# Performance work log

Measured on AMD Instinct MI355X. Metric: run time of the kernel, lower is better.

Reference implementation:

```python
import jax, jax.numpy as jnp
import numpy as np

B, L, K, D, S = 8, 1024, 1024, 128, 16  # batch, nodes, eigvecs, d_model(=d_inner), d_state
ABAR_EPS = 1e-3
BN_EPS = 1e-5


def setup_inputs() -> dict:
    key = jax.random.key(0)
    ks = jax.random.split(key, 10)
    x = jax.random.normal(ks[0], (B, L, D), jnp.float32)
    attn_mask = jnp.ones((B, L), jnp.bool_)
    EigVecs = jax.random.normal(ks[1], (B, L, K), jnp.float32)
    EigVals = jax.random.uniform(ks[2], (B, K), jnp.float32)
    # BatchNorm1d (eval mode) params
    bn_gamma = jnp.ones((D,), jnp.float32)
    bn_beta = jnp.zeros((D,), jnp.float32)
    bn_mean = jnp.zeros((D,), jnp.float32)
    bn_var = jnp.ones((D,), jnp.float32)
    # in_proj Linear(D, 2*D)
    W_in = jax.random.normal(ks[3], (D, 2 * D), jnp.float32) / np.float32(np.sqrt(D))
    b_in = jnp.zeros((2 * D,), jnp.float32)
    # SSM params
    log_Delta = np.float32(np.log(1e-3)) + np.float32(np.log(0.1) - np.log(1e-3)) * jax.random.uniform(ks[4], (1, D), jnp.float32)
    Bp = 0.01 * jax.random.normal(ks[5], (1, D, S), jnp.float32)
    Cp = 0.01 * jax.random.normal(ks[6], (1, D, S), jnp.float32)
    log_A_real = jnp.log(0.5 * jnp.ones((D, S), jnp.float32))
    A_imag = jnp.pi * jnp.broadcast_to(jnp.arange(D, dtype=jnp.float32)[:, None], (D, S))
    # out_proj Linear(D, D)
    W_out = jax.random.normal(ks[7], (D, D), jnp.float32) / np.float32(np.sqrt(D))
    b_out = jnp.zeros((D,), jnp.float32)
    return {
        "x": x, "attn_mask": attn_mask, "EigVecs": EigVecs, "EigVals": EigVals,
        "bn_gamma": bn_gamma, "bn_beta": bn_beta, "bn_mean": bn_mean, "bn_var": bn_var,
        "W_in": W_in, "b_in": b_in, "log_Delta": log_Delta, "Bp": Bp, "Cp": Cp,
        "log_A_real": log_A_real, "A_imag": A_imag, "W_out": W_out, "b_out": b_out,
    }


def reference(x, attn_mask, EigVecs, EigVals, bn_gamma, bn_beta, bn_mean, bn_var,
              W_in, b_in, log_Delta, Bp, Cp, log_A_real, A_imag, W_out, b_out):
    # --- eig preprocessing ---
    ev = 1.0 - EigVals[:, :, None, None]            # (B,K,1,1)
    ev = jnp.nan_to_num(ev)
    Q = jnp.nan_to_num(EigVecs)                      # (B,L,K)
    Q = Q / jnp.linalg.norm(Q, axis=-1, keepdims=True)
    Q = jnp.nan_to_num(Q)
    # --- in_proj: BatchNorm1d (eval) + Linear ---
    xb = (x - bn_mean) * (bn_gamma / jnp.sqrt(bn_var + BN_EPS)) + bn_beta
    h = xb @ W_in + b_in                             # (B,L,2D)
    x1, z = jnp.split(h, 2, axis=-1)                 # split [d_model, d_model]
    u = x1 * jax.nn.silu(z)                          # (B,L,D)
    # --- discretized SSM params ---
    delta = jnp.exp(log_Delta)                       # (1,D)
    A = -jnp.exp(log_A_real) + 1j * A_imag           # (D,S) complex
    Abar = jnp.exp(-ABAR_EPS + delta[..., None] * A) # (1,D,S) complex
    Bbar = delta[..., None] * Bp                     # (1,D,S)
    # --- graph Fourier transform ---
    QTX = jnp.einsum('blk,bld->bkd', Q, u)           # (B,K,D)
    QTXB = QTX[..., None] * Bbar                     # (B,K,D,S)
    lamA = ev * Abar[:, None]                        # (B,K,D,S) complex
    lamQ = jnp.real(lamA / (1.0 - lamA) * QTXB)      # A_complex & not BC_complex -> .real
    # --- inverse transform + C reduction (fused) ---
    yssm = jnp.einsum('blk,bkds,ds->bld', Q, lamQ, Cp[0])  # (B,L,D)
    y = jax.nn.silu(yssm) @ W_out + b_out
    return y
```

## Files before the change

kernel.cpp:

```cpp
#include <hip/hip_runtime.h>
#include <math.h>

#define B_ 8
#define L_ 1024
#define K_ 1024
#define D_ 128
#define S_ 16
#define DS_ (D_ * S_)
#define NIT_ 16

typedef short bf16x8 __attribute__((ext_vector_type(8)));
typedef float f32x4 __attribute__((ext_vector_type(4)));
typedef __attribute__((address_space(1))) const unsigned int gu32;
typedef __attribute__((address_space(3))) unsigned int lu32;

__device__ inline unsigned short f2bf(float f) {
    unsigned int u = __float_as_uint(f);
    u = (u + 0x7fffu + ((u >> 16) & 1u)) >> 16;
    return (unsigned short)u;
}
__device__ inline float bf2f(unsigned short h) {
    return __uint_as_float(((unsigned int)h) << 16);
}

__device__ inline size_t bswz(int b, int c, int n) {
    return ((((size_t)b * 32 + (c >> 5)) * 4 + ((c >> 3) & 3)) * 128 + n) * 8;
}

__global__ __launch_bounds__(256) void k_pre(
    const float* __restrict__ E, const float* __restrict__ x,
    const float* __restrict__ g, const float* __restrict__ beta,
    const float* __restrict__ mean, const float* __restrict__ var,
    const float* __restrict__ W_in, const float* __restrict__ b_in,
    const float* __restrict__ log_Delta, const float* __restrict__ Bp,
    const float* __restrict__ Cp, const float* __restrict__ log_A_real,
    const float* __restrict__ A_imag, const float* __restrict__ W_out,
    float* __restrict__ rn_out, float* __restrict__ par,
    unsigned short* __restrict__ woH, unsigned short* __restrict__ woL,
    unsigned short* __restrict__ uswH, unsigned short* __restrict__ uswL) {
    __shared__ unsigned short xbh[4][16][32], xbl[4][16][32];
    __shared__ float szs[16][132];
    __shared__ float us[16][132];
    __shared__ float rsum[16];
    __shared__ float rnS[16];
    int bx = blockIdx.x;
    int row0 = bx * 16;
    int t = threadIdx.x;
    if (bx < 8) {
        int i = bx * 256 + t;
        int d = i >> 4, s = i & 15;
        double delta = exp((double)log_Delta[d]);
        double Are = -exp((double)log_A_real[i]);
        double Aim = (double)A_imag[i];
        double mag = exp(-1e-3 + delta * Are);
        double ang = delta * Aim;
        int o = s * D_ + d;
        par[o]           = (float)(mag * cos(ang));
        par[DS_ + o]     = (float)(mag * sin(ang));
        par[2 * DS_ + o] = (float)(delta * (double)Bp[i] * (double)Cp[i]);
    }
    if (bx >= 8 && bx < 12) {
        int kc = bx - 8;
        #pragma unroll
        for (int j = 0; j < 16; ++j) {
            int s = t * 16 + j;
            int ws = s >> 10, nt = (s >> 9) & 1, ln = (s >> 3) & 63, ii = s & 7;
            int row = kc * 32 + (ln >> 4) * 8 + ii;
            int col = ws * 32 + nt * 16 + (ln & 15);
            float wv = W_out[row * 128 + col];
            unsigned short h = f2bf(wv);
            woH[kc * 4096 + s] = h;
            woL[kc * 4096 + s] = f2bf(wv - bf2f(h));
        }
    }
    {
        int r = t >> 4, tt = t & 15;
        const float4* Ep = (const float4*)(E + (size_t)(row0 + r) * K_);
        float s = 0.f;
        #pragma unroll
        for (int i = 0; i < 16; ++i) {
            float4 v = Ep[tt + i * 16];
            s += v.x * v.x + v.y * v.y + v.z * v.z + v.w * v.w;
        }
        s += __shfl_xor(s, 8, 64);
        s += __shfl_xor(s, 4, 64);
        s += __shfl_xor(s, 2, 64);
        s += __shfl_xor(s, 1, 64);
        if (tt == 0) rsum[r] = s;
    }
    #pragma unroll
    for (int p = 0; p < 8; ++p) {
        int idx = t + p * 256;
        int dd = idx & 127, r = idx >> 7;
        float sc = g[dd] / sqrtf(var[dd] + 1e-5f);
        float v = (x[(size_t)(row0 + r) * D_ + dd] - mean[dd]) * sc + beta[dd];
        unsigned short h = f2bf(v);
        xbh[dd >> 5][r][dd & 31] = h;
        xbl[dd >> 5][r][dd & 31] = f2bf(v - bf2f(h));
    }
    __syncthreads();
    if (t < 16) {
        float rv = 1.0f / sqrtf(rsum[t]);
        rnS[t] = rv;
        rn_out[row0 + t] = rv;
    }
    __syncthreads();
    int wave = t >> 6, lane = t & 63;
    int fr = lane & 15, q = lane >> 4;
    f32x4 acc[4];
    #pragma unroll
    for (int ct = 0; ct < 4; ++ct) acc[ct] = (f32x4){0.f, 0.f, 0.f, 0.f};
    #pragma unroll
    for (int c = 0; c < 4; ++c) {
        bf16x8 ah = *(const bf16x8*)&xbh[c][fr][q * 8];
        bf16x8 al = *(const bf16x8*)&xbl[c][fr][q * 8];
        #pragma unroll
        for (int ct = 0; ct < 4; ++ct) {
            int col = wave * 64 + ct * 16 + fr;
            bf16x8 bh, bl;
            #pragma unroll
            for (int i = 0; i < 8; ++i) {
                float wv = W_in[(c * 32 + q * 8 + i) * 256 + col];
                unsigned short h = f2bf(wv);
                bh[i] = (short)h;
                bl[i] = (short)f2bf(wv - bf2f(h));
            }
            acc[ct] = __builtin_amdgcn_mfma_f32_16x16x32_bf16(ah, bh, acc[ct], 0, 0, 0);
            acc[ct] = __builtin_amdgcn_mfma_f32_16x16x32_bf16(ah, bl, acc[ct], 0, 0, 0);
            acc[ct] = __builtin_amdgcn_mfma_f32_16x16x32_bf16(al, bh, acc[ct], 0, 0, 0);
        }
    }
    if (wave >= 2) {
        #pragma unroll
        for (int ct = 0; ct < 4; ++ct) {
            int cz = (wave - 2) * 64 + ct * 16 + fr;
            float b2v = b_in[128 + cz];
            #pragma unroll
            for (int r = 0; r < 4; ++r) {
                float z = acc[ct][r] + b2v;
                float sig = 1.0f / (1.0f + __expf(-z));
                szs[q * 4 + r][cz] = z * sig;
            }
        }
    }
    __syncthreads();
    if (wave < 2) {
        #pragma unroll
        for (int ct = 0; ct < 4; ++ct) {
            int cx = wave * 64 + ct * 16 + fr;
            float b1v = b_in[cx];
            #pragma unroll
            for (int r = 0; r < 4; ++r) {
                int row = q * 4 + r;
                float x1 = acc[ct][r] + b1v;
                us[row][cx] = rnS[row] * x1 * szs[row][cx];
            }
        }
    }
    __syncthreads();
    int j = t & 127, half = t >> 7;
    bf16x8 hv, lv;
    #pragma unroll
    for (int r = 0; r < 8; ++r) {
        float uv = us[half * 8 + r][j];
        unsigned short h = f2bf(uv);
        hv[r] = (short)h;
        lv[r] = (short)f2bf(uv - bf2f(h));
    }
    int b = row0 >> 10;
    int l0 = (row0 & 1023) + half * 8;
    size_t off = bswz(b, l0, j);
    *(bf16x8*)&uswH[off] = hv;
    *(bf16x8*)&uswL[off] = lv;
}

#define STAGE_B(itS, nb)                                                        \
    _Pragma("unroll")                                                           \
    for (int j2 = 0; j2 < 4; ++j2) {                                            \
        int s = wave * 4 + j2;                         \
        int cts = s >> 4, s2 = s & 15;                                          \
        int qq = s2 & 3, nh = (s2 >> 2) & 1, hl = s2 >> 3;                      \
        size_t src0 = (size_t)((itS) * 2 + cts) * 4096;                         \
        const unsigned short* src =                                             \
            (hl ? BbL : BbH) + src0 + ((size_t)qq * 128 + nh * 64 + lane) * 8;  \
        unsigned short* dst =                                                   \
            (hl ? &sBl[nb][cts][0] : &sBh[nb][cts][0]) + qq * 1032 + nh * 512;  \
        __builtin_amdgcn_global_load_lds((gu32*)src, (lu32*)dst, 16, 0, 0);     \
    }

#define G1_WRITE_A(nb, v0, v1, v2, v3)                                           \
    {                                                                            \
        unsigned short h0 = f2bf(v0), h1 = f2bf(v1);                             \
        unsigned short l0 = f2bf((v0) - bf2f(h0)), l1 = f2bf((v1) - bf2f(h1));   \
        *(unsigned int*)&sAh[nb][0][aoff] = (unsigned)h0 | ((unsigned)h1 << 16); \
        *(unsigned int*)&sAl[nb][0][aoff] = (unsigned)l0 | ((unsigned)l1 << 16); \
        unsigned short h2 = f2bf(v2), h3 = f2bf(v3);                             \
        unsigned short l2 = f2bf((v2) - bf2f(h2)), l3 = f2bf((v3) - bf2f(h3));   \
        *(unsigned int*)&sAh[nb][1][aoff] = (unsigned)h2 | ((unsigned)h3 << 16); \
        *(unsigned int*)&sAl[nb][1][aoff] = (unsigned)l2 | ((unsigned)l3 << 16); \
    }

#define MFMA_PHASE(aB, cB)                                                       \
    {                                                                            \
        __builtin_amdgcn_s_setprio(1);                                           \
        bf16x8 ah[2], al[2], bh[2], bl[2];                                       \
        _Pragma("unroll")                                                        \
        for (int mt = 0; mt < 2; ++mt) {                                         \
            int row = mt * 16 + fr;                                              \
            int p = (q + (row >> 3)) & 3;                                        \
            int offA = row * 40 + p * 8;                                         \
            ah[mt] = *(const bf16x8*)&sAh[aB][kh][offA];                         \
            al[mt] = *(const bf16x8*)&sAl[aB][kh][offA];                         \
        }                                                                        \
        _Pragma("unroll")                                                        \
        for (int nt = 0; nt < 2; ++nt) {                                         \
            int offB = q * 1032 + (wn + nt * 16 + fr) * 8;                       \
            bh[nt] = *(const bf16x8*)&sBh[cB][kh][offB];                         \
            bl[nt] = *(const bf16x8*)&sBl[cB][kh][offB];                         \
        }                                                                        \
        _Pragma("unroll")                                                        \
        for (int mt = 0; mt < 2; ++mt)                                           \
            _Pragma("unroll")                                                    \
            for (int nt = 0; nt < 2; ++nt) {                                     \
                acc[mt][nt] = __builtin_amdgcn_mfma_f32_16x16x32_bf16(ah[mt], bh[nt], acc[mt][nt], 0, 0, 0); \
                acc[mt][nt] = __builtin_amdgcn_mfma_f32_16x16x32_bf16(ah[mt], bl[nt], acc[mt][nt], 0, 0, 0); \
                acc[mt][nt] = __builtin_amdgcn_mfma_f32_16x16x32_bf16(al[mt], bh[nt], acc[mt][nt], 0, 0, 0); \
            }                                                                    \
        __builtin_amdgcn_s_setprio(0);                                           \
    }

__global__ __launch_bounds__(512, 2) void k_g1(
    const float* __restrict__ E,
    const unsigned short* __restrict__ BH, const unsigned short* __restrict__ BL,
    const float* __restrict__ EigVals, const float* __restrict__ par,
    unsigned short* __restrict__ GswH, unsigned short* __restrict__ GswL) {
    __shared__ alignas(16) unsigned short sAh[2][2][1280], sAl[2][2][1280];
    __shared__ alignas(16) unsigned short sBh[3][2][4128], sBl[3][2][4128];
    __shared__ float evS[32];
    int bx = blockIdx.x;
    int b = bx & 7;
    int m0 = (bx >> 3) * 32;
    const float* Ab = E + (size_t)b * (1024 * 1024);
    const unsigned short* BbH = BH + (size_t)b * 131072;
    const unsigned short* BbL = BL + (size_t)b * 131072;
    int t = threadIdx.x;
    int wave = t >> 6, lane = t & 63;
    int fr = lane & 15, q = lane >> 4;
    int kh = wave & 1;
    int wn = (wave >> 1) * 32;
    int am = t & 31, jj = t >> 5;
    int ag = jj >> 2;
    int arot = (ag + (am >> 3)) & 3;
    int aoff = am * 40 + arot * 8 + ((2 * jj) & 7);
    if (t < 32) evS[t] = 1.0f - EigVals[b * 1024 + m0 + t];
    f32x4 acc[2][2];
    #pragma unroll
    for (int mt = 0; mt < 2; ++mt)
        #pragma unroll
        for (int nt = 0; nt < 2; ++nt)
            acc[mt][nt] = (f32x4){0.f, 0.f, 0.f, 0.f};

    {
        STAGE_B(0, 0);
        STAGE_B(1, 1);
        float v0 = Ab[(size_t)(2 * jj) * 1024 + m0 + am];
        float v1 = Ab[(size_t)(2 * jj + 1) * 1024 + m0 + am];
        float v2 = Ab[(size_t)(32 + 2 * jj) * 1024 + m0 + am];
        float v3 = Ab[(size_t)(32 + 2 * jj + 1) * 1024 + m0 + am];
        G1_WRITE_A(0, v0, v1, v2, v3);
        asm volatile("s_waitcnt vmcnt(0) lgkmcnt(0)" ::: "memory");
        __builtin_amdgcn_s_barrier();
        asm volatile("" ::: "memory");
    }

    for (int it = 0; it < NIT_; ++it) {
        int cB = it % 3;
        int fB = (it + 2) % 3;
        int aB = it & 1, naB = aB ^ 1;
        float v0 = 0.f, v1 = 0.f, v2 = 0.f, v3 = 0.f;
        if (it + 1 < NIT_) {
            int cb = (it + 1) * 64;
            v0 = Ab[(size_t)(cb + 2 * jj) * 1024 + m0 + am];
            v1 = Ab[(size_t)(cb + 2 * jj + 1) * 1024 + m0 + am];
            v2 = Ab[(size_t)(cb + 32 + 2 * jj) * 1024 + m0 + am];
            v3 = Ab[(size_t)(cb + 32 + 2 * jj + 1) * 1024 + m0 + am];
        }
        if (it + 2 < NIT_) STAGE_B(it + 2, fB);
        MFMA_PHASE(aB, cB)
        if (it + 1 < NIT_) G1_WRITE_A(naB, v0, v1, v2, v3);
        asm volatile("s_waitcnt lgkmcnt(0)" ::: "memory");
        __builtin_amdgcn_s_barrier();
        asm volatile("" ::: "memory");
    }

    float (*Gs)[132] = (float (*)[132])(&sBh[0][0][0]);
    if (kh == 0) {
        #pragma unroll
        for (int mt = 0; mt < 2; ++mt)
            #pragma unroll
            for (int nt = 0; nt < 2; ++nt) {
                int col = wn + nt * 16 + fr;
                #pragma unroll
                for (int r = 0; r < 4; ++r)
                    Gs[mt * 16 + q * 4 + r][col] = acc[mt][nt][r];
            }
    }
    __syncthreads();
    if (kh == 1) {
        #pragma unroll
        for (int mt = 0; mt < 2; ++mt)
            #pragma unroll
            for (int nt = 0; nt < 2; ++nt) {
                int col = wn + nt * 16 + fr;
                #pragma unroll
                for (int r = 0; r < 4; ++r)
                    Gs[mt * 16 + q * 4 + r][col] += acc[mt][nt][r];
            }
    }
    __syncthreads();
    {
        int col = t & 127, rowg = t >> 7;
        float arr[S_], aii[S_], ccc[S_];
        #pragma unroll
        for (int ss = 0; ss < S_; ++ss) {
            arr[ss] = par[ss * D_ + col];
            aii[ss] = par[DS_ + ss * D_ + col];
            ccc[ss] = par[2 * DS_ + ss * D_ + col];
        }
        #pragma unroll
        for (int i = 0; i < 8; ++i) {
            int row = rowg * 8 + i;
            float ev = evS[row];
            float w = 0.f;
            #pragma unroll
            for (int ss = 0; ss < S_; ++ss) {
                float a = ev * arr[ss], bi = ev * aii[ss];
                float oma = 1.0f - a;
                float b2 = bi * bi;
                float num = fmaf(a, oma, -b2);
                float den = fmaf(oma, oma, b2);
                float rr = __builtin_amdgcn_rcpf(den);
                rr = rr * (2.0f - den * rr);
                w = fmaf(ccc[ss], num * rr, w);
            }
            Gs[row][col] *= w;
        }
    }
    __syncthreads();
    {
        int d = t & 127, kg = t >> 7;
        bf16x8 hv, lv;
        #pragma unroll
        for (int i = 0; i < 8; ++i) {
            float v = Gs[kg * 8 + i][d];
            unsigned short h = f2bf(v);
            hv[i] = (short)h;
            lv[i] = (short)f2bf(v - bf2f(h));
        }
        int ct = m0 >> 5;
        size_t off = (((size_t)(b * 32 + ct) * 4 + kg) * 128 + d) * 8;
        *(bf16x8*)&GswH[off] = hv;
        *(bf16x8*)&GswL[off] = lv;
    }
}

#define G2_WRITE_A(nb, va)                                                       \
    {                                                                            \
        unsigned short h0 = f2bf((va).x), h1 = f2bf((va).y);                     \
        unsigned short h2 = f2bf((va).z), h3 = f2bf((va).w);                     \
        unsigned short l0 = f2bf((va).x - bf2f(h0)), l1 = f2bf((va).y - bf2f(h1));\
        unsigned short l2 = f2bf((va).z - bf2f(h2)), l3 = f2bf((va).w - bf2f(h3));\
        *(uint2*)&sAh[nb][chunk][aoff] =                                         \
            (uint2){(unsigned)h0 | ((unsigned)h1 << 16),                         \
                    (unsigned)h2 | ((unsigned)h3 << 16)};                        \
        *(uint2*)&sAl[nb][chunk][aoff] =                                         \
            (uint2){(unsigned)l0 | ((unsigned)l1 << 16),                         \
                    (unsigned)l2 | ((unsigned)l3 << 16)};                        \
    }

__global__ __launch_bounds__(512, 2) void k_g2(
    const float* __restrict__ E,
    const unsigned short* __restrict__ BH, const unsigned short* __restrict__ BL,
    const float* __restrict__ rn,
    const unsigned short* __restrict__ woH, const unsigned short* __restrict__ woL,
    const float* __restrict__ b_out, float* __restrict__ y) {
    __shared__ alignas(16) unsigned short sAh[2][2][1280], sAl[2][2][1280];
    __shared__ alignas(16) unsigned short sBh[3][2][4128], sBl[3][2][4128];
    __shared__ float rnS[32];
    int bx = blockIdx.x;
    int b = bx & 7;
    int m0 = (bx >> 3) * 32;
    const float* Ab = E + (size_t)b * (1024 * 1024);
    const unsigned short* BbH = BH + (size_t)b * 131072;
    const unsigned short* BbL = BL + (size_t)b * 131072;
    int t = threadIdx.x;
    int wave = t >> 6, lane = t & 63;
    int fr = lane & 15, q = lane >> 4;
    int kh = wave & 1;
    int wn = (wave >> 1) * 32;
    int am = t >> 4, c4 = (t & 15) * 4;
    int chunk = c4 >> 5, cw = c4 & 31;
    int ag = cw >> 3;
    int arot = (ag + (am >> 3)) & 3;
    int aoff = am * 40 + arot * 8 + (cw & 7);
    if (t < 32) rnS[t] = rn[b * 1024 + m0 + t];
    f32x4 acc[2][2];
    #pragma unroll
    for (int mt = 0; mt < 2; ++mt)
        #pragma unroll
        for (int nt = 0; nt < 2; ++nt)
            acc[mt][nt] = (f32x4){0.f, 0.f, 0.f, 0.f};

    {
        STAGE_B(0, 0);
        STAGE_B(1, 1);
        float4 va = *(const float4*)&Ab[(size_t)(m0 + am) * 1024 + c4];
        G2_WRITE_A(0, va);
        asm volatile("s_waitcnt vmcnt(0) lgkmcnt(0)" ::: "memory");
        __builtin_amdgcn_s_barrier();
        asm volatile("" ::: "memory");
    }

    for (int it = 0; it < NIT_; ++it) {
        int cB = it % 3;
        int fB = (it + 2) % 3;
        int aB = it & 1, naB = aB ^ 1;
        float4 va = (float4){0.f, 0.f, 0.f, 0.f};
        if (it + 1 < NIT_)
            va = *(const float4*)&Ab[(size_t)(m0 + am) * 1024 + (it + 1) * 64 + c4];
        if (it + 2 < NIT_) STAGE_B(it + 2, fB);
        MFMA_PHASE(aB, cB)
        if (it + 1 < NIT_) G2_WRITE_A(naB, va);
        asm volatile("s_waitcnt lgkmcnt(0)" ::: "memory");
        __builtin_amdgcn_s_barrier();
        asm volatile("" ::: "memory");
    }

    float (*Ysf)[132] = (float (*)[132])(&sBh[0][0][0]);
    if (kh == 0) {
        #pragma unroll
        for (int mt = 0; mt < 2; ++mt)
            #pragma unroll
            for (int nt = 0; nt < 2; ++nt) {
                int col = wn + nt * 16 + fr;
                #pragma unroll
                for (int r = 0; r < 4; ++r)
                    Ysf[mt * 16 + q * 4 + r][col] = acc[mt][nt][r];
            }
    }
    __syncthreads();
    if (kh == 1) {
        #pragma unroll
        for (int mt = 0; mt < 2; ++mt)
            #pragma unroll
            for (int nt = 0; nt < 2; ++nt) {
                int col = wn + nt * 16 + fr;
                #pragma unroll
                for (int r = 0; r < 4; ++r)
                    Ysf[mt * 16 + q * 4 + r][col] += acc[mt][nt][r];
            }
    }
    __syncthreads();
    unsigned short (*ysh)[32][40] = (unsigned short (*)[32][40])(&sBl[0][0][0]);
    unsigned short (*ysl)[32][40] = (unsigned short (*)[32][40])(&sBl[0][0][0] + 5120);
    {
        int col = t & 127, rowg = t >> 7;
        #pragma unroll
        for (int i = 0; i < 8; ++i) {
            int row = rowg * 8 + i;
            float v = Ysf[row][col] * rnS[row];
            float sig = 1.0f / (1.0f + __expf(-v));
            float u = v * sig;
            unsigned short h = f2bf(u);
            ysh[col >> 5][row][col & 31] = h;
            ysl[col >> 5][row][col & 31] = f2bf(u - bf2f(h));
        }
    }
    __syncthreads();
    {
        int mh = wave & 1, ws = wave >> 1;
        const bf16x8* WH = (const bf16x8*)woH;
        const bf16x8* WL = (const bf16x8*)woL;
        f32x4 a2[2];
        a2[0] = (f32x4){0.f, 0.f, 0.f, 0.f};
        a2[1] = (f32x4){0.f, 0.f, 0.f, 0.f};
        #pragma unroll
        for (int kc = 0; kc < 4; ++kc) {
            bf16x8 ah = *(const bf16x8*)&ysh[kc][mh * 16 + fr][q * 8];
            bf16x8 al = *(const bf16x8*)&ysl[kc][mh * 16 + fr][q * 8];
            #pragma unroll
            for (int nt = 0; nt < 2; ++nt) {
                bf16x8 bh = WH[((kc * 4 + ws) * 2 + nt) * 64 + lane];
                bf16x8 bl = WL[((kc * 4 + ws) * 2 + nt) * 64 + lane];
                a2[nt] = __builtin_amdgcn_mfma_f32_16x16x32_bf16(ah, bh, a2[nt], 0, 0, 0);
                a2[nt] = __builtin_amdgcn_mfma_f32_16x16x32_bf16(ah, bl, a2[nt], 0, 0, 0);
                a2[nt] = __builtin_amdgcn_mfma_f32_16x16x32_bf16(al, bh, a2[nt], 0, 0, 0);
            }
        }
        #pragma unroll
        for (int nt = 0; nt < 2; ++nt) {
            int col = ws * 32 + nt * 16 + fr;
            float bo = b_out[col];
            #pragma unroll
            for (int r = 0; r < 4; ++r) {
                int row = mh * 16 + q * 4 + r;
                y[((size_t)b * 1024 + m0 + row) * 128 + col] = a2[nt][r] + bo;
            }
        }
    }
}

extern "C" void kernel_launch(void* const* d_in, const int* in_sizes, int n_in,
                              void* d_out, int out_size, void* d_ws, size_t ws_size,
                              hipStream_t stream) {
    const float* x          = (const float*)d_in[0];
    const float* EigVecs    = (const float*)d_in[2];
    const float* EigVals    = (const float*)d_in[3];
    const float* bn_gamma   = (const float*)d_in[4];
    const float* bn_beta    = (const float*)d_in[5];
    const float* bn_mean    = (const float*)d_in[6];
    const float* bn_var     = (const float*)d_in[7];
    const float* W_in       = (const float*)d_in[8];
    const float* b_in       = (const float*)d_in[9];
    const float* log_Delta  = (const float*)d_in[10];
    const float* Bp         = (const float*)d_in[11];
    const float* Cp         = (const float*)d_in[12];
    const float* log_A_real = (const float*)d_in[13];
    const float* A_imag     = (const float*)d_in[14];
    const float* W_out      = (const float*)d_in[15];
    const float* b_out      = (const float*)d_in[16];

    float* y = (float*)d_out;
    char* w = (char*)d_ws;
    float* rn            = (float*)(w);
    float* par           = (float*)(w + 32768);
    unsigned short* woH  = (unsigned short*)(w + 57344);
    unsigned short* woL  = (unsigned short*)(w + 90112);
    unsigned short* uswH = (unsigned short*)(w + 131072);
    unsigned short* uswL = (unsigned short*)(w + 131072 + (1u << 21));
    unsigned short* GswH = (unsigned short*)(w + 131072 + 2 * (1u << 21));
    unsigned short* GswL = (unsigned short*)(w + 131072 + 3 * (1u << 21));

    k_pre<<<dim3(B_ * L_ / 16), dim3(256), 0, stream>>>(
        EigVecs, x, bn_gamma, bn_beta, bn_mean, bn_var, W_in, b_in,
        log_Delta, Bp, Cp, log_A_real, A_imag, W_out, rn, par, woH, woL,
        uswH, uswL);
    k_g1<<<dim3(256), dim3(512), 0, stream>>>(
        EigVecs, uswH, uswL, EigVals, par, GswH, GswL);
    k_g2<<<dim3(256), dim3(512), 0, stream>>>(
        EigVecs, GswH, GswL, rn, woH, woL, b_out, y);
}
```

Baseline: 154.5 us.

## Pre-split W_in to bf16 hi/lo once and pair rational terms in weight

Adds a small kernel that converts W_in into pre-swizzled bf16 high/low fragments once per call. k_pre then loads these fragments directly instead of having each of its 512 blocks reload and split the fp32 weights. Separately, the per-state rational weight sum is rewritten so two terms share one reciprocal, using num = oma - den, which halves the rcp and Newton-step work. The cost is an extra kernel launch, extra workspace, and slightly different rounding in the weight sum.

```diff
diff --git a/kernel.cpp b/kernel.cpp
--- a/kernel.cpp
+++ b/kernel.cpp
@@ -27,11 +27,32 @@
     return ((((size_t)b * 32 + (c >> 5)) * 4 + ((c >> 3) & 3)) * 128 + n) * 8;
 }
 
+__global__ __launch_bounds__(256) void k_w(
+    const float* __restrict__ W_in,
+    unsigned short* __restrict__ wiH, unsigned short* __restrict__ wiL) {
+    int g = blockIdx.x * 256 + threadIdx.x;
+    int lane = g & 63, rest = g >> 6;
+    int ct = rest & 3, wv = (rest >> 2) & 3, c = rest >> 4;
+    int rbase = c * 32 + (lane >> 4) * 8;
+    int col = wv * 64 + ct * 16 + (lane & 15);
+    bf16x8 hv, lv;
+    #pragma unroll
+    for (int i = 0; i < 8; ++i) {
+        float wvl = W_in[(rbase + i) * 256 + col];
+        unsigned short h = f2bf(wvl);
+        hv[i] = (short)h;
+        lv[i] = (short)f2bf(wvl - bf2f(h));
+    }
+    *(bf16x8*)&wiH[(size_t)g * 8] = hv;
+    *(bf16x8*)&wiL[(size_t)g * 8] = lv;
+}
+
 __global__ __launch_bounds__(256) void k_pre(
     const float* __restrict__ E, const float* __restrict__ x,
     const float* __restrict__ g, const float* __restrict__ beta,
     const float* __restrict__ mean, const float* __restrict__ var,
-    const float* __restrict__ W_in, const float* __restrict__ b_in,
+    const unsigned short* __restrict__ wiH, const unsigned short* __restrict__ wiL,
+    const float* __restrict__ b_in,
     const float* __restrict__ log_Delta, const float* __restrict__ Bp,
     const float* __restrict__ Cp, const float* __restrict__ log_A_real,
     const float* __restrict__ A_imag, const float* __restrict__ W_out,
@@ -107,6 +128,8 @@
     __syncthreads();
     int wave = t >> 6, lane = t & 63;
     int fr = lane & 15, q = lane >> 4;
+    const bf16x8* WIH = (const bf16x8*)wiH;
+    const bf16x8* WIL = (const bf16x8*)wiL;
     f32x4 acc[4];
     #pragma unroll
     for (int ct = 0; ct < 4; ++ct) acc[ct] = (f32x4){0.f, 0.f, 0.f, 0.f};
@@ -116,15 +139,9 @@
         bf16x8 al = *(const bf16x8*)&xbl[c][fr][q * 8];
         #pragma unroll
         for (int ct = 0; ct < 4; ++ct) {
-            int col = wave * 64 + ct * 16 + fr;
-            bf16x8 bh, bl;
-            #pragma unroll
-            for (int i = 0; i < 8; ++i) {
-                float wv = W_in[(c * 32 + q * 8 + i) * 256 + col];
-                unsigned short h = f2bf(wv);
-                bh[i] = (short)h;
-                bl[i] = (short)f2bf(wv - bf2f(h));
-            }
+            int idx = ((c * 4 + wave) * 4 + ct) * 64 + lane;
+            bf16x8 bh = WIH[idx];
+            bf16x8 bl = WIL[idx];
             acc[ct] = __builtin_amdgcn_mfma_f32_16x16x32_bf16(ah, bh, acc[ct], 0, 0, 0);
             acc[ct] = __builtin_amdgcn_mfma_f32_16x16x32_bf16(ah, bl, acc[ct], 0, 0, 0);
             acc[ct] = __builtin_amdgcn_mfma_f32_16x16x32_bf16(al, bh, acc[ct], 0, 0, 0);
@@ -333,15 +350,27 @@
             float ev = evS[row];
             float w = 0.f;
             #pragma unroll
-            for (int ss = 0; ss < S_; ++ss) {
-                float a = ev * arr[ss], bi = ev * aii[ss];
-                float oma = 1.0f - a;
-                float b2 = bi * bi;
-                float num = fmaf(a, oma, -b2);
-                float den = fmaf(oma, oma, b2);
-                float rr = __builtin_amdgcn_rcpf(den);
-                rr = rr * (2.0f - den * rr);
-                w = fmaf(ccc[ss], num * rr, w);
+            for (int sp = 0; sp < 8; ++sp) {
+                float n0, n1, d0, d1;
+                {
+                    int ss = sp * 2;
+                    float a = ev * arr[ss], bi = ev * aii[ss];
+                    float oma = 1.0f - a;
+                    d0 = fmaf(oma, oma, bi * bi);
+                    n0 = ccc[ss] * (oma - d0);
+                }
+                {
+                    int ss = sp * 2 + 1;
+                    float a = ev * arr[ss], bi = ev * aii[ss];
+                    float oma = 1.0f - a;
+                    d1 = fmaf(oma, oma, bi * bi);
+                    n1 = ccc[ss] * (oma - d1);
+                }
+                float num = fmaf(n0, d1, n1 * d0);
+                float dpr = d0 * d1;
+                float rr = __builtin_amdgcn_rcpf(dpr);
+                rr = rr * (2.0f - dpr * rr);
+                w = fmaf(num, rr, w);
             }
             Gs[row][col] *= w;
         }
@@ -536,13 +565,16 @@
     float* par           = (float*)(w + 32768);
     unsigned short* woH  = (unsigned short*)(w + 57344);
     unsigned short* woL  = (unsigned short*)(w + 90112);
-    unsigned short* uswH = (unsigned short*)(w + 131072);
-    unsigned short* uswL = (unsigned short*)(w + 131072 + (1u << 21));
-    unsigned short* GswH = (unsigned short*)(w + 131072 + 2 * (1u << 21));
-    unsigned short* GswL = (unsigned short*)(w + 131072 + 3 * (1u << 21));
-
+    unsigned short* wiH  = (unsigned short*)(w + 131072);
+    unsigned short* wiL  = (unsigned short*)(w + 196608);
+    unsigned short* uswH = (unsigned short*)(w + 262144);
+    unsigned short* uswL = (unsigned short*)(w + 262144 + (1u << 21));
+    unsigned short* GswH = (unsigned short*)(w + 262144 + 2 * (1u << 21));
+    unsigned short* GswL = (unsigned short*)(w + 262144 + 3 * (1u << 21));
+
+    k_w<<<dim3(16), dim3(256), 0, stream>>>(W_in, wiH, wiL);
     k_pre<<<dim3(B_ * L_ / 16), dim3(256), 0, stream>>>(
-        EigVecs, x, bn_gamma, bn_beta, bn_mean, bn_var, W_in, b_in,
+        EigVecs, x, bn_gamma, bn_beta, bn_mean, bn_var, wiH, wiL, b_in,
         log_Delta, Bp, Cp, log_A_real, A_imag, W_out, rn, par, woH, woL,
         uswH, uswL);
     k_g1<<<dim3(256), dim3(512), 0, stream>>>(
```

Result: no change. 152.3 us, median of 2 (-1.4%).
